# Kernel tuning notes

Hardware: AMD Instinct MI355X
Metric: run time of the kernel (lower is better)

The kernel has to match this reference:

```python
import jax, jax.numpy as jnp
import numpy as np

L, C, H, DH, S, N, B = 12, 768, 12, 64, 2, 577, 1
ALT_START, ROPE_START = 0, 0
OUT_LAYERS = (2, 5, 8, 11)
EPS = 1e-6


def _ln(x, w, b):
    m = jnp.mean(x, axis=-1, keepdims=True)
    v = jnp.var(x, axis=-1, keepdims=True)
    return (x - m) * jax.lax.rsqrt(v + EPS) * w + b


def _rms(x, w):
    return x * jax.lax.rsqrt(jnp.mean(x * x, axis=-1, keepdims=True) + EPS) * w


def _rot_half(x):
    h = x.shape[-1] // 2
    return jnp.concatenate([-x[..., h:], x[..., :h]], axis=-1)


def _rope(t, cos, sin):
    # t: [Bf, H, N, DH]; cos/sin: [N, DH] split into y/x halves
    h = t.shape[-1] // 2
    tv, th = t[..., :h], t[..., h:]
    cy, cx = cos[..., :h], cos[..., h:]
    sy, sx = sin[..., :h], sin[..., h:]
    return jnp.concatenate([tv * cy + _rot_half(tv) * sy,
                            th * cx + _rot_half(th) * sx], axis=-1)


def _block(xf, cos, sin, kv, p):
    (qkv_w, qkv_b, qn, kn, pw, pb, g1, g2,
     n1w, n1b, n2w, n2b, f1w, f1b, f2w, f2b) = p
    Bf, Nn, Cc = xf.shape
    h = _ln(xf, n1w, n1b)
    qkv = (jnp.einsum('bnc,oc->bno', h, qkv_w) + qkv_b)
    qkv = qkv.reshape(Bf, Nn, 3, H, DH).transpose(2, 0, 3, 1, 4)
    q, k, v = qkv[0], qkv[1], qkv[2]
    q, k = _rms(q, qn), _rms(k, kn)
    q, k = _rope(q, cos, sin), _rope(k, cos, sin)
    bias = ((1.0 - kv) * (-10000.0))[:, None, None, :]
    scores = jnp.einsum('bhqd,bhkd->bhqk', q, k) / np.sqrt(DH) + bias
    attn = jax.nn.softmax(scores, axis=-1)
    o = jnp.einsum('bhqk,bhkd->bhqd', attn, v).transpose(0, 2, 1, 3).reshape(Bf, Nn, Cc)
    o = jnp.einsum('bnc,oc->bno', o, pw) + pb
    xf = xf + g1 * o
    h2 = _ln(xf, n2w, n2b)
    m = jax.nn.gelu(jnp.einsum('bnc,oc->bno', h2, f1w) + f1b, approximate=False)
    m = jnp.einsum('bnd,od->bno', m, f2w) + f2b
    return xf + g2 * m


def _forward(x, rope_cos_local, rope_sin_local, rope_cos_global, rope_sin_global,
             key_valid_local, key_valid_global, camera_token,
             qkv_w, qkv_b, q_norm_w, k_norm_w, proj_w, proj_b,
             ls1_gamma, ls2_gamma, norm1_w, norm1_b, norm2_w, norm2_b,
             fc1_w, fc1_b, fc2_w, fc2_b, final_norm_w, final_norm_b):
    Bb, Ss, Nn, Cc = x.shape
    stacked = (qkv_w, qkv_b, q_norm_w, k_norm_w, proj_w, proj_b, ls1_gamma,
               ls2_gamma, norm1_w, norm1_b, norm2_w, norm2_b, fc1_w, fc1_b,
               fc2_w, fc2_b)
    local_x = x
    outputs = []
    cam_token_out = None
    max_out = max(OUT_LAYERS)
    for i in range(L):
        if i == ALT_START:
            ref = jnp.broadcast_to(camera_token[:, :1], (Bb, 1, Cc))
            src = jnp.broadcast_to(camera_token[:, 1:], (Bb, Ss - 1, Cc))
            x = x.at[:, :, 0].set(jnp.concatenate([ref, src], axis=1))
        p = tuple(a[i] for a in stacked)
        is_global = (i % 2 == 1)  # alt_start == 0
        if is_global:
            xf = x.reshape(Bb, Ss * Nn, Cc)
            xf = _block(xf, rope_cos_global, rope_sin_global, key_valid_global, p)
            x = xf.reshape(Bb, Ss, Nn, Cc)
        else:
            xf = x.reshape(Bb * Ss, Nn, Cc)
            xf = _block(xf, rope_cos_local, rope_sin_local, key_valid_local, p)
            x = xf.reshape(Bb, Ss, Nn, Cc)
            local_x = x
        if i in OUT_LAYERS:
            out_x = jnp.concatenate([local_x, x], axis=-1)  # cat_token=True
            outputs.append(out_x)
            if i == max_out:
                cam_token_out = out_x[:, :, 0]
    processed = []
    for o in outputs:
        o = jnp.concatenate([o[..., :Cc], _ln(o[..., Cc:], final_norm_w, final_norm_b)], axis=-1)
        o = o[..., 1:, :]  # drop cam/cls token (num_register_tokens=0)
        processed.append(o)
    return (processed[0], processed[1], processed[2], processed[3], cam_token_out)


def setup_inputs() -> dict:
    key = jax.random.key(0)
    ks = iter(jax.random.split(key, 40))
    rn = lambda sh, s=0.02: jax.random.normal(next(ks), sh, dtype=jnp.float32) * s
    two_pi = 2.0 * np.pi
    ang_l = jax.random.uniform(next(ks), (N, DH), dtype=jnp.float32) * two_pi
    ang_g = jax.random.uniform(next(ks), (S * N, DH), dtype=jnp.float32) * two_pi
    kv_l = (jax.random.uniform(next(ks), (B * S, N)) > 0.1).astype(jnp.float32)
    kv_g = (jax.random.uniform(next(ks), (B, S * N)) > 0.1).astype(jnp.float32)
    return {
        'x': rn((B, S, N, C), 1.0),
        'rope_cos_local': jnp.cos(ang_l), 'rope_sin_local': jnp.sin(ang_l),
        'rope_cos_global': jnp.cos(ang_g), 'rope_sin_global': jnp.sin(ang_g),
        'key_valid_local': kv_l, 'key_valid_global': kv_g,
        'camera_token': rn((1, 2, C)),
        'qkv_w': rn((L, 3 * C, C)), 'qkv_b': rn((L, 3 * C)),
        'q_norm_w': jnp.ones((L, DH), jnp.float32),
        'k_norm_w': jnp.ones((L, DH), jnp.float32),
        'proj_w': rn((L, C, C)), 'proj_b': rn((L, C)),
        'ls1_gamma': rn((L, C), 0.1), 'ls2_gamma': rn((L, C), 0.1),
        'norm1_w': jnp.ones((L, C), jnp.float32), 'norm1_b': jnp.zeros((L, C), jnp.float32),
        'norm2_w': jnp.ones((L, C), jnp.float32), 'norm2_b': jnp.zeros((L, C), jnp.float32),
        'fc1_w': rn((L, 4 * C, C)), 'fc1_b': rn((L, 4 * C)),
        'fc2_w': rn((L, C, 4 * C)), 'fc2_b': rn((L, C)),
        'final_norm_w': jnp.ones((C,), jnp.float32),
        'final_norm_b': jnp.zeros((C,), jnp.float32),
    }


def reference(x, rope_cos_local, rope_sin_local, rope_cos_global, rope_sin_global,
              key_valid_local, key_valid_global, camera_token,
              qkv_w, qkv_b, q_norm_w, k_norm_w, proj_w, proj_b,
              ls1_gamma, ls2_gamma, norm1_w, norm1_b, norm2_w, norm2_b,
              fc1_w, fc1_b, fc2_w, fc2_b, final_norm_w, final_norm_b):
    return _forward(x, rope_cos_local, rope_sin_local, rope_cos_global, rope_sin_global,
                    key_valid_local, key_valid_global, camera_token,
                    qkv_w, qkv_b, q_norm_w, k_norm_w, proj_w, proj_b,
                    ls1_gamma, ls2_gamma, norm1_w, norm1_b, norm2_w, norm2_b,
                    fc1_w, fc1_b, fc2_w, fc2_b, final_norm_w, final_norm_b)
```

## Files before the change

### kernel.cpp

```cpp
#include <hip/hip_runtime.h>
#include <hip/hip_bf16.h>
#include <math.h>

typedef __hip_bfloat16 bf16;
typedef __attribute__((ext_vector_type(4))) float floatx4;
typedef __attribute__((ext_vector_type(8))) short shortx8;

#define T_TOK 1154
#define C_DIM 768
#define H_HEADS 12
#define NLOC 577
#define OUT_PER 1769472

#define NQ  1769472ull
#define NP  589824ull
#define NF1 2359296ull
#define NF2 2359296ull
#define NWTOT 7077888ull
#define WQ  0ull
#define WP  1769472ull
#define WF1 2359296ull
#define WF2 4718592ull

static __device__ __forceinline__ float b2f(bf16 v) { return __bfloat162float(v); }
static __device__ __forceinline__ bf16 f2b(float v) { return __float2bfloat16(v); }

static __device__ __forceinline__ void gload16(const bf16* g, short* l) {
    __builtin_amdgcn_global_load_lds(
        (__attribute__((address_space(1))) void*)(void*)g,
        (__attribute__((address_space(3))) void*)(void*)l, 16, 0, 0);
}

__global__ void k_init(const float* __restrict__ xin, const float* __restrict__ cam,
                       float* __restrict__ xF, int total) {
    int idx = blockIdx.x * 256 + threadIdx.x;
    if (idx >= total) return;
    int t = idx / C_DIM, c = idx - t * C_DIM;
    int s = t / NLOC, n = t - s * NLOC;
    float v = (n == 0) ? cam[s * C_DIM + c] : xin[idx];
    xF[idx] = v;
}

__global__ void k_cast(const float* __restrict__ src, bf16* __restrict__ dst, int total) {
    int idx = blockIdx.x * 256 + threadIdx.x;
    if (idx < total) dst[idx] = f2b(src[idx]);
}

__global__ __launch_bounds__(256) void k_wconv_all(
    const float* __restrict__ wq, const float* __restrict__ wp,
    const float* __restrict__ wf1, const float* __restrict__ wf2,
    bf16* __restrict__ dst, int nL) {
    size_t total = (size_t)nL * NWTOT / 8;
    for (size_t i = (size_t)blockIdx.x * 256 + threadIdx.x; i < total;
         i += (size_t)gridDim.x * 256) {
        size_t e = i * 8;
        size_t layer = e / NWTOT, off = e - layer * NWTOT;
        const float* src; size_t o2;
        if (off < WP)       { src = wq  + layer * NQ;  o2 = off; }
        else if (off < WF1) { src = wp  + layer * NP;  o2 = off - WP; }
        else if (off < WF2) { src = wf1 + layer * NF1; o2 = off - WF1; }
        else                { src = wf2 + layer * NF2; o2 = off - WF2; }
        float4 a = *(const float4*)(src + o2);
        float4 b = *(const float4*)(src + o2 + 4);
        bf16 pk[8];
        pk[0] = f2b(a.x); pk[1] = f2b(a.y); pk[2] = f2b(a.z); pk[3] = f2b(a.w);
        pk[4] = f2b(b.x); pk[5] = f2b(b.y); pk[6] = f2b(b.z); pk[7] = f2b(b.w);
        *(shortx8*)(dst + e) = *(shortx8*)pk;
    }
}

__global__ __launch_bounds__(256) void k_ln(const float* __restrict__ xF,
                                            const float* __restrict__ w, const float* __restrict__ b,
                                            bf16* __restrict__ out) {
    int t = blockIdx.x;
    const float* xr = xF + (size_t)t * C_DIM;
    float s = 0.f, s2 = 0.f;
    for (int c = threadIdx.x; c < C_DIM; c += 256) { float v = xr[c]; s += v; s2 += v * v; }
    __shared__ float red[8];
    for (int o = 32; o; o >>= 1) { s += __shfl_xor(s, o, 64); s2 += __shfl_xor(s2, o, 64); }
    int wv = threadIdx.x >> 6;
    if ((threadIdx.x & 63) == 0) { red[wv] = s; red[4 + wv] = s2; }
    __syncthreads();
    s = red[0] + red[1] + red[2] + red[3];
    s2 = red[4] + red[5] + red[6] + red[7];
    float mean = s * (1.0f / C_DIM);
    float var = s2 * (1.0f / C_DIM) - mean * mean;
    if (var < 0.f) var = 0.f;
    float inv = rsqrtf(var + 1e-6f);
    bf16* orow = out + (size_t)t * C_DIM;
    for (int c = threadIdx.x; c < C_DIM; c += 256) {
        float v = (xr[c] - mean) * inv * w[c] + b[c];
        orow[c] = f2b(v);
    }
}

template<int BM, int BN, int MODE>
__global__ __launch_bounds__(256) void k_gemmT(
    const bf16* __restrict__ A, const bf16* __restrict__ Bt,
    const float* __restrict__ bias, const float* __restrict__ gamma,
    bf16* __restrict__ outB, float* __restrict__ xio,
    int M, int N, int K, int mB, int kS) {
    constexpr int FM = BM / 32;
    constexpr int FN = BN / 32;
    __shared__ short At[2][BM * 64];
    __shared__ short Bs[2][BN * 64];
    int nwg = gridDim.x;
    int lid = blockIdx.x;
    int qd = nwg >> 3, rm = nwg & 7;
    int xcd = lid & 7, pos = lid >> 3;
    int lid2 = (xcd < rm ? xcd * (qd + 1) : rm * (qd + 1) + (xcd - rm) * qd) + pos;
    int mI = lid2 % mB;
    int rest = lid2 / mB;
    int nB = N / BN;
    int nI = rest % nB;
    int kI = rest / nB;
    int m0 = mI * BM, n0 = nI * BN;
    int Ksub = K / kS;
    int kOff = kI * Ksub;
    int tid = threadIdx.x;
    int w = tid >> 6, lane = tid & 63;
    int lr = lane & 15, lq = lane >> 4;
    int wm = w & 1, wn = w >> 1;
    int srow = tid >> 3;
    int schk = tid & 7;
    floatx4 acc[FM][FN] = {};

    auto stage = [&](int buf, int k0) {
        #pragma unroll
        for (int j = 0; j < BM / 32; j++) {
            int r = j * 32 + srow;
            int ar = m0 + r; if (ar >= M) ar = M - 1;
            int gs = schk ^ (r & 7);
            gload16(A + (size_t)ar * K + kOff + k0 + gs * 8, &At[buf][r * 64 + schk * 8]);
        }
        #pragma unroll
        for (int j = 0; j < BN / 32; j++) {
            int r = j * 32 + srow;
            int gs = schk ^ (r & 7);
            gload16(Bt + (size_t)(n0 + r) * K + kOff + k0 + gs * 8, &Bs[buf][r * 64 + schk * 8]);
        }
    };

    int nt = Ksub / 64;
    stage(0, 0);
    __syncthreads();
    int cur = 0;
    int rx = lr & 7;
    for (int t = 0; t < nt; ++t) {
        if (t + 1 < nt) stage(cur ^ 1, (t + 1) * 64);
        #pragma unroll
        for (int kk = 0; kk < 2; kk++) {
            shortx8 af[FM], bg[FN];
            #pragma unroll
            for (int mi = 0; mi < FM; mi++) {
                int rowl = wm * (BM / 2) + mi * 16 + lr;
                af[mi] = *(const shortx8*)&At[cur][rowl * 64 + ((kk * 4 + lq) ^ rx) * 8];
            }
            #pragma unroll
            for (int ni = 0; ni < FN; ni++) {
                int rowl = wn * (BN / 2) + ni * 16 + lr;
                bg[ni] = *(const shortx8*)&Bs[cur][rowl * 64 + ((kk * 4 + lq) ^ rx) * 8];
            }
            #pragma unroll
            for (int mi = 0; mi < FM; mi++)
                #pragma unroll
                for (int ni = 0; ni < FN; ni++)
                    acc[mi][ni] = __builtin_amdgcn_mfma_f32_16x16x32_bf16(af[mi], bg[ni], acc[mi][ni], 0, 0, 0);
        }
        __syncthreads();
        cur ^= 1;
    }

    #pragma unroll
    for (int mi = 0; mi < FM; mi++) {
        #pragma unroll
        for (int ni = 0; ni < FN; ni++) {
            int cc = n0 + wn * (BN / 2) + ni * 16 + lr;
            #pragma unroll
            for (int rg = 0; rg < 4; rg++) {
                int rr = m0 + wm * (BM / 2) + mi * 16 + lq * 4 + rg;
                if (rr < M) {
                    float u = acc[mi][ni][rg];
                    if (MODE == 2) {
                        u += (kI == 0) ? bias[cc] : 0.f;
                        float contrib = gamma[cc] * u;
                        if (kS > 1) atomicAdd(&xio[(size_t)rr * N + cc], contrib);
                        else        xio[(size_t)rr * N + cc] += contrib;
                    } else if (MODE == 1) {
                        u += bias[cc];
                        float g = 0.5f * u * (1.0f + erff(u * 0.70710678118f));
                        outB[(size_t)rr * N + cc] = f2b(g);
                    } else {
                        u += bias[cc];
                        outB[(size_t)rr * N + cc] = f2b(u);
                    }
                }
            }
        }
    }
}

__global__ __launch_bounds__(256) void k_qkprep(
    const bf16* __restrict__ qkv,
    const float* __restrict__ qnw, const float* __restrict__ knw,
    const float* __restrict__ ctab, const float* __restrict__ stab, int posMod,
    bf16* __restrict__ qh, bf16* __restrict__ kh, bf16* __restrict__ vh) {
    int gw = blockIdx.x * 4 + (threadIdx.x >> 6);
    int lane = threadIdx.x & 63;
    if (gw >= T_TOK * H_HEADS) return;
    int t = gw / H_HEADS, h = gw - t * H_HEADS;
    size_t base = (size_t)t * 2304 + h * 64 + lane;
    float q = b2f(qkv[base]), k = b2f(qkv[base + 768]), v = b2f(qkv[base + 1536]);
    float sq = q * q, sk = k * k;
    for (int o = 32; o; o >>= 1) { sq += __shfl_xor(sq, o, 64); sk += __shfl_xor(sk, o, 64); }
    q = q * rsqrtf(sq * (1.0f / 64.0f) + 1e-6f) * qnw[lane];
    k = k * rsqrtf(sk * (1.0f / 64.0f) + 1e-6f) * knw[lane];
    int pos = t % posMod;
    float cv = ctab[pos * 64 + lane];
    float sv = stab[pos * 64 + lane];
    float qp = __shfl_xor(q, 16, 64);
    float kp = __shfl_xor(k, 16, 64);
    float sgn = (lane & 16) ? 1.0f : -1.0f;
    float qo = q * cv + sgn * qp * sv;
    float ko = k * cv + sgn * kp * sv;
    size_t oidx = ((size_t)h * T_TOK + t) * 64 + lane;
    qh[oidx] = f2b(qo);
    kh[oidx] = f2b(ko);
    vh[oidx] = f2b(v);
}

__global__ __launch_bounds__(256) void k_attn2(
    const bf16* __restrict__ qh, const bf16* __restrict__ kh, const bf16* __restrict__ vh,
    const float* __restrict__ mask, bf16* __restrict__ out, int nk) {
    __shared__ short Ks[64 * 72];
    __shared__ short Vs[64 * 72];
    __shared__ short Ps[4][16 * 72];
    __shared__ float bias_s[64];
    int h = blockIdx.y;
    int base = blockIdx.z * nk;
    int tid = threadIdx.x;
    int wv = tid >> 6, lane = tid & 63;
    int lr = lane & 15, lq = lane >> 4;
    int q0 = blockIdx.x * 64 + wv * 16;
    shortx8 qf[2];
    {
        int qr = q0 + lr; if (qr >= nk) qr = nk - 1;
        const bf16* qp = qh + ((size_t)h * T_TOK + base + qr) * 64 + lq * 8;
        qf[0] = *(const shortx8*)(qp);
        qf[1] = *(const shortx8*)(qp + 32);
    }
    float mrow[4] = {-3.0e38f, -3.0e38f, -3.0e38f, -3.0e38f};
    float lrow[4] = {0.f, 0.f, 0.f, 0.f};
    floatx4 accO[4] = {};
    short* pbuf = &Ps[wv][0];
    int nkt = (nk + 63) >> 6;
    for (int kt0 = 0; kt0 < nkt; kt0++) {
        int kbase = kt0 * 64;
        __syncthreads();
        for (int idx = tid; idx < 64 * 8; idx += 256) {
            int kr = idx >> 3, seg = idx & 7;
            int gk = kbase + kr;
            shortx8 v = {};
            if (gk < nk) v = *(const shortx8*)(kh + ((size_t)h * T_TOK + base + gk) * 64 + seg * 8);
            *(shortx8*)&Ks[kr * 72 + seg * 8] = v;
        }
        for (int idx = tid; idx < 64 * 8; idx += 256) {
            int kr = idx & 63, seg = idx >> 6;
            int gk = kbase + kr;
            shortx8 v = {};
            if (gk < nk) v = *(const shortx8*)(vh + ((size_t)h * T_TOK + base + gk) * 64 + seg * 8);
            bf16* vb = (bf16*)&v;
            #pragma unroll
            for (int j = 0; j < 8; j++)
                Vs[(seg * 8 + j) * 72 + kr] = *(short*)&vb[j];
        }
        if (tid < 64) {
            int gk = kbase + tid;
            bias_s[tid] = (gk < nk) ? (1.0f - mask[base + gk]) * -10000.0f : -30000.0f;
        }
        __syncthreads();
        floatx4 s[4];
        #pragma unroll
        for (int nt = 0; nt < 4; nt++) {
            floatx4 accS = {};
            shortx8 k0 = *(const shortx8*)&Ks[(nt * 16 + lr) * 72 + lq * 8];
            shortx8 k1 = *(const shortx8*)&Ks[(nt * 16 + lr) * 72 + 32 + lq * 8];
            accS = __builtin_amdgcn_mfma_f32_16x16x32_bf16(qf[0], k0, accS, 0, 0, 0);
            accS = __builtin_amdgcn_mfma_f32_16x16x32_bf16(qf[1], k1, accS, 0, 0, 0);
            s[nt] = accS;
        }
        float tmax[4] = {-3.0e38f, -3.0e38f, -3.0e38f, -3.0e38f};
        #pragma unroll
        for (int nt = 0; nt < 4; nt++) {
            float bv = bias_s[nt * 16 + lr];
            #pragma unroll
            for (int rg = 0; rg < 4; rg++) {
                float sv = s[nt][rg] * 0.125f + bv;
                s[nt][rg] = sv;
                tmax[rg] = fmaxf(tmax[rg], sv);
            }
        }
        #pragma unroll
        for (int rg = 0; rg < 4; rg++) {
            for (int o = 1; o < 16; o <<= 1) tmax[rg] = fmaxf(tmax[rg], __shfl_xor(tmax[rg], o, 16));
        }
        float fac[4], tsum[4] = {0.f, 0.f, 0.f, 0.f};
        #pragma unroll
        for (int rg = 0; rg < 4; rg++) {
            float mn = fmaxf(mrow[rg], tmax[rg]);
            fac[rg] = __expf(mrow[rg] - mn);
            mrow[rg] = mn;
        }
        #pragma unroll
        for (int nt = 0; nt < 4; nt++) {
            #pragma unroll
            for (int rg = 0; rg < 4; rg++) {
                float e = __expf(s[nt][rg] - mrow[rg]);
                s[nt][rg] = e;
                tsum[rg] += e;
            }
        }
        #pragma unroll
        for (int rg = 0; rg < 4; rg++) {
            for (int o = 1; o < 16; o <<= 1) tsum[rg] += __shfl_xor(tsum[rg], o, 16);
            lrow[rg] = lrow[rg] * fac[rg] + tsum[rg];
        }
        #pragma unroll
        for (int dt = 0; dt < 4; dt++)
            #pragma unroll
            for (int rg = 0; rg < 4; rg++) accO[dt][rg] *= fac[rg];
        #pragma unroll
        for (int nt = 0; nt < 4; nt++) {
            #pragma unroll
            for (int rg = 0; rg < 4; rg++) {
                bf16 pv = f2b(s[nt][rg]);
                pbuf[(lq * 4 + rg) * 72 + nt * 16 + lr] = *(short*)&pv;
            }
        }
        #pragma unroll
        for (int ks = 0; ks < 2; ks++) {
            shortx8 pf = *(const shortx8*)&pbuf[lr * 72 + ks * 32 + lq * 8];
            #pragma unroll
            for (int dt = 0; dt < 4; dt++) {
                shortx8 vf = *(const shortx8*)&Vs[(dt * 16 + lr) * 72 + ks * 32 + lq * 8];
                accO[dt] = __builtin_amdgcn_mfma_f32_16x16x32_bf16(pf, vf, accO[dt], 0, 0, 0);
            }
        }
    }
    float invl[4];
    #pragma unroll
    for (int rg = 0; rg < 4; rg++) invl[rg] = 1.0f / lrow[rg];
    #pragma unroll
    for (int rg = 0; rg < 4; rg++) {
        int qr = q0 + lq * 4 + rg;
        if (qr < nk) {
            bf16* orow = out + (size_t)(base + qr) * C_DIM + h * 64 + lr;
            #pragma unroll
            for (int dt = 0; dt < 4; dt++)
                orow[dt * 16] = f2b(accO[dt][rg] * invl[rg]);
        }
    }
}

__global__ __launch_bounds__(256) void k_output(
    const float* __restrict__ xF, const bf16* __restrict__ lxB,
    const float* __restrict__ fw, const float* __restrict__ fb, float* __restrict__ dst) {
    int b = blockIdx.x;
    int s = b / 576, nn = b - s * 576;
    int t = s * NLOC + nn + 1;
    const float* xr = xF + (size_t)t * C_DIM;
    float sum = 0.f, s2 = 0.f;
    for (int c = threadIdx.x; c < C_DIM; c += 256) { float v = xr[c]; sum += v; s2 += v * v; }
    __shared__ float red[8];
    for (int o = 32; o; o >>= 1) { sum += __shfl_xor(sum, o, 64); s2 += __shfl_xor(s2, o, 64); }
    if ((threadIdx.x & 63) == 0) { red[threadIdx.x >> 6] = sum; red[4 + (threadIdx.x >> 6)] = s2; }
    __syncthreads();
    sum = red[0] + red[1] + red[2] + red[3];
    s2 = red[4] + red[5] + red[6] + red[7];
    float mean = sum * (1.0f / C_DIM);
    float var = s2 * (1.0f / C_DIM) - mean * mean;
    if (var < 0.f) var = 0.f;
    float inv = rsqrtf(var + 1e-6f);
    float* orow = dst + (size_t)b * 1536;
    const bf16* lr = lxB + (size_t)t * C_DIM;
    for (int c = threadIdx.x; c < C_DIM; c += 256) {
        orow[c] = b2f(lr[c]);
        float v = (xr[c] - mean) * inv * fw[c] + fb[c];
        orow[768 + c] = v;
    }
}

__global__ void k_cam(const float* __restrict__ xF, const bf16* __restrict__ lxB,
                      float* __restrict__ dst) {
    for (int idx = threadIdx.x; idx < 2 * 1536; idx += 256) {
        int s = idx / 1536, c = idx - s * 1536;
        int t = s * NLOC;
        float v = (c < 768) ? b2f(lxB[(size_t)t * 768 + c]) : xF[(size_t)t * 768 + (c - 768)];
        dst[idx] = v;
    }
}

extern "C" void kernel_launch(void* const* d_in, const int* in_sizes, int n_in,
                              void* d_out, int out_size, void* d_ws, size_t ws_size,
                              hipStream_t stream) {
    const float* xin  = (const float*)d_in[0];
    const float* rcl  = (const float*)d_in[1];
    const float* rsl  = (const float*)d_in[2];
    const float* rcg  = (const float*)d_in[3];
    const float* rsg  = (const float*)d_in[4];
    const float* kvl  = (const float*)d_in[5];
    const float* kvg  = (const float*)d_in[6];
    const float* cam  = (const float*)d_in[7];
    const float* qkvw = (const float*)d_in[8];
    const float* qkvb = (const float*)d_in[9];
    const float* qnw  = (const float*)d_in[10];
    const float* knw  = (const float*)d_in[11];
    const float* pw   = (const float*)d_in[12];
    const float* pb   = (const float*)d_in[13];
    const float* ls1  = (const float*)d_in[14];
    const float* ls2  = (const float*)d_in[15];
    const float* n1w  = (const float*)d_in[16];
    const float* n1b  = (const float*)d_in[17];
    const float* n2w  = (const float*)d_in[18];
    const float* n2b  = (const float*)d_in[19];
    const float* f1w  = (const float*)d_in[20];
    const float* f1b  = (const float*)d_in[21];
    const float* f2w  = (const float*)d_in[22];
    const float* f2b_ = (const float*)d_in[23];
    const float* fnw  = (const float*)d_in[24];
    const float* fnb  = (const float*)d_in[25];

    char* ws = (char*)d_ws;
    const size_t TC = (size_t)T_TOK * C_DIM;
    float* xF  = (float*)ws; ws += TC * 4;
    bf16* bufA = (bf16*)ws;  ws += (size_t)T_TOK * 3072 * 2;
    bf16* qhb  = (bf16*)ws;  ws += TC * 2;
    bf16* khb  = (bf16*)ws;  ws += TC * 2;
    bf16* vhb  = (bf16*)ws;  ws += TC * 2;
    bf16* hbuf = (bf16*)ws;  ws += TC * 2;
    bf16* lxB  = (bf16*)ws;  ws += TC * 2;
    bf16* wAll = (bf16*)ws;
    size_t usedBase = (size_t)(ws - (char*)d_ws);
    bool bigW = ws_size >= usedBase + 12ull * NWTOT * 2ull;
    (void)n_in; (void)in_sizes; (void)out_size;

    float* out_b = (float*)d_out;

    k_init<<<(int)((TC + 255) / 256), 256, 0, stream>>>(xin, cam, xF, (int)TC);
    if (bigW)
        k_wconv_all<<<4096, 256, 0, stream>>>(qkvw, pw, f1w, f2w, wAll, 12);

    int outIdx = 0;
    for (int i = 0; i < 12; i++) {
        bool isGlobal = (i & 1);
        bf16* wL;
        if (bigW) {
            wL = wAll + (size_t)i * NWTOT;
        } else {
            k_wconv_all<<<2048, 256, 0, stream>>>(
                qkvw + (size_t)i * NQ, pw + (size_t)i * NP,
                f1w + (size_t)i * NF1, f2w + (size_t)i * NF2, wAll, 1);
            wL = wAll;
        }
        k_ln<<<T_TOK, 256, 0, stream>>>(xF, n1w + (size_t)i * 768, n1b + (size_t)i * 768, hbuf);
        k_gemmT<64, 64, 3><<<684, 256, 0, stream>>>(hbuf, wL + WQ,
            qkvb + (size_t)i * 2304, nullptr, bufA, nullptr, T_TOK, 2304, 768, 19, 1);
        k_qkprep<<<(T_TOK * H_HEADS) / 4, 256, 0, stream>>>(bufA,
            qnw + (size_t)i * 64, knw + (size_t)i * 64,
            isGlobal ? rcg : rcl, isGlobal ? rsg : rsl, isGlobal ? 1154 : 577,
            qhb, khb, vhb);
        if (isGlobal)
            k_attn2<<<dim3(19, 12, 1), 256, 0, stream>>>(qhb, khb, vhb, kvg, hbuf, 1154);
        else
            k_attn2<<<dim3(10, 12, 2), 256, 0, stream>>>(qhb, khb, vhb, kvl, hbuf, 577);
        k_gemmT<64, 64, 2><<<456, 256, 0, stream>>>(hbuf, wL + WP,
            pb + (size_t)i * 768, ls1 + (size_t)i * 768, nullptr, xF, T_TOK, 768, 768, 19, 2);
        k_ln<<<T_TOK, 256, 0, stream>>>(xF, n2w + (size_t)i * 768, n2b + (size_t)i * 768, hbuf);
        k_gemmT<64, 64, 1><<<912, 256, 0, stream>>>(hbuf, wL + WF1,
            f1b + (size_t)i * 3072, nullptr, bufA, nullptr, T_TOK, 3072, 768, 19, 1);
        k_gemmT<64, 64, 2><<<912, 256, 0, stream>>>(bufA, wL + WF2,
            f2b_ + (size_t)i * 768, ls2 + (size_t)i * 768, nullptr, xF, T_TOK, 768, 3072, 19, 4);

        if (i == 2 || i == 4 || i == 8 || i == 10)
            k_cast<<<(int)((TC + 255) / 256), 256, 0, stream>>>(xF, lxB, (int)TC);

        if (i == 2 || i == 5 || i == 8 || i == 11) {
            k_output<<<1152, 256, 0, stream>>>(xF, lxB, fnw, fnb, out_b + (size_t)outIdx * OUT_PER);
            if (i == 11)
                k_cam<<<1, 256, 0, stream>>>(xF, lxB, out_b + 4ull * OUT_PER);
            outIdx++;
        }
    }
}
```

Baseline: 1.917 ms.

## Fuse QK norm and RoPE into QKV GEMM, prefetch attention K/V, reshape weight conversion

Replaces the separate qkprep kernel with a dedicated QKV GEMM whose epilogue applies bias, per-head RMS norm (cross-warp reduction through shared memory) and RoPE, then writes head-major q/k/v directly. This removes the intermediate bf16 QKV buffer round trip and one launch per layer. The attention kernel now register-prefetches the next K/V tile and mask bias while the current tile is being processed. The weight-conversion kernel is also changed to a 3D grid with one element group per thread, which drops the grid-stride loop and per-element layer/type division.

```diff
diff --git a/kernel.cpp b/kernel.cpp
--- a/kernel.cpp
+++ b/kernel.cpp
@@ -46,27 +46,27 @@
     if (idx < total) dst[idx] = f2b(src[idx]);
 }
 
-__global__ __launch_bounds__(256) void k_wconv_all(
+__global__ __launch_bounds__(256) void k_wconv3(
     const float* __restrict__ wq, const float* __restrict__ wp,
     const float* __restrict__ wf1, const float* __restrict__ wf2,
-    bf16* __restrict__ dst, int nL) {
-    size_t total = (size_t)nL * NWTOT / 8;
-    for (size_t i = (size_t)blockIdx.x * 256 + threadIdx.x; i < total;
-         i += (size_t)gridDim.x * 256) {
-        size_t e = i * 8;
-        size_t layer = e / NWTOT, off = e - layer * NWTOT;
-        const float* src; size_t o2;
-        if (off < WP)       { src = wq  + layer * NQ;  o2 = off; }
-        else if (off < WF1) { src = wp  + layer * NP;  o2 = off - WP; }
-        else if (off < WF2) { src = wf1 + layer * NF1; o2 = off - WF1; }
-        else                { src = wf2 + layer * NF2; o2 = off - WF2; }
-        float4 a = *(const float4*)(src + o2);
-        float4 b = *(const float4*)(src + o2 + 4);
-        bf16 pk[8];
-        pk[0] = f2b(a.x); pk[1] = f2b(a.y); pk[2] = f2b(a.z); pk[3] = f2b(a.w);
-        pk[4] = f2b(b.x); pk[5] = f2b(b.y); pk[6] = f2b(b.z); pk[7] = f2b(b.w);
-        *(shortx8*)(dst + e) = *(shortx8*)pk;
-    }
+    bf16* __restrict__ dst) {
+    int typ = blockIdx.y, layer = blockIdx.z;
+    size_t cnt, off;
+    const float* srcb;
+    if (typ == 0)      { cnt = NQ;  off = WQ;  srcb = wq; }
+    else if (typ == 1) { cnt = NP;  off = WP;  srcb = wp; }
+    else if (typ == 2) { cnt = NF1; off = WF1; srcb = wf1; }
+    else               { cnt = NF2; off = WF2; srcb = wf2; }
+    size_t e = ((size_t)blockIdx.x * 256 + threadIdx.x) * 8;
+    if (e >= cnt) return;
+    const float* src = srcb + (size_t)layer * cnt + e;
+    bf16* d = dst + (size_t)layer * NWTOT + off + e;
+    float4 a = *(const float4*)(src);
+    float4 b = *(const float4*)(src + 4);
+    bf16 pk[8];
+    pk[0] = f2b(a.x); pk[1] = f2b(a.y); pk[2] = f2b(a.z); pk[3] = f2b(a.w);
+    pk[4] = f2b(b.x); pk[5] = f2b(b.y); pk[6] = f2b(b.z); pk[7] = f2b(b.w);
+    *(shortx8*)d = *(shortx8*)pk;
 }
 
 __global__ __launch_bounds__(256) void k_ln(const float* __restrict__ xF,
@@ -200,33 +200,152 @@
     }
 }
 
-__global__ __launch_bounds__(256) void k_qkprep(
-    const bf16* __restrict__ qkv,
+__global__ __launch_bounds__(256) void k_gemmQKV(
+    const bf16* __restrict__ A, const bf16* __restrict__ Bt,
+    const float* __restrict__ bias,
     const float* __restrict__ qnw, const float* __restrict__ knw,
     const float* __restrict__ ctab, const float* __restrict__ stab, int posMod,
-    bf16* __restrict__ qh, bf16* __restrict__ kh, bf16* __restrict__ vh) {
-    int gw = blockIdx.x * 4 + (threadIdx.x >> 6);
-    int lane = threadIdx.x & 63;
-    if (gw >= T_TOK * H_HEADS) return;
-    int t = gw / H_HEADS, h = gw - t * H_HEADS;
-    size_t base = (size_t)t * 2304 + h * 64 + lane;
-    float q = b2f(qkv[base]), k = b2f(qkv[base + 768]), v = b2f(qkv[base + 1536]);
-    float sq = q * q, sk = k * k;
-    for (int o = 32; o; o >>= 1) { sq += __shfl_xor(sq, o, 64); sk += __shfl_xor(sk, o, 64); }
-    q = q * rsqrtf(sq * (1.0f / 64.0f) + 1e-6f) * qnw[lane];
-    k = k * rsqrtf(sk * (1.0f / 64.0f) + 1e-6f) * knw[lane];
-    int pos = t % posMod;
-    float cv = ctab[pos * 64 + lane];
-    float sv = stab[pos * 64 + lane];
-    float qp = __shfl_xor(q, 16, 64);
-    float kp = __shfl_xor(k, 16, 64);
-    float sgn = (lane & 16) ? 1.0f : -1.0f;
-    float qo = q * cv + sgn * qp * sv;
-    float ko = k * cv + sgn * kp * sv;
-    size_t oidx = ((size_t)h * T_TOK + t) * 64 + lane;
-    qh[oidx] = f2b(qo);
-    kh[oidx] = f2b(ko);
-    vh[oidx] = f2b(v);
+    bf16* __restrict__ qh, bf16* __restrict__ kh, bf16* __restrict__ vh,
+    int M, int K) {
+    constexpr int BM = 64, BN = 64, FM = 2, FN = 2;
+    const int N = 2304, mB = 19;
+    __shared__ short At[2][BM * 64];
+    __shared__ short Bs[2][BN * 64];
+    __shared__ float ssqS[2][64];
+    int nwg = gridDim.x;
+    int lid = blockIdx.x;
+    int qd = nwg >> 3, rm = nwg & 7;
+    int xcd = lid & 7, pos = lid >> 3;
+    int lid2 = (xcd < rm ? xcd * (qd + 1) : rm * (qd + 1) + (xcd - rm) * qd) + pos;
+    int mI = lid2 % mB;
+    int nI = lid2 / mB;
+    int m0 = mI * BM, n0 = nI * BN;
+    int tid = threadIdx.x;
+    int w = tid >> 6, lane = tid & 63;
+    int lr = lane & 15, lq = lane >> 4;
+    int wm = w & 1, wn = w >> 1;
+    int srow = tid >> 3, schk = tid & 7;
+    floatx4 acc[FM][FN] = {};
+
+    auto stage = [&](int buf, int k0) {
+        #pragma unroll
+        for (int j = 0; j < BM / 32; j++) {
+            int r = j * 32 + srow;
+            int ar = m0 + r; if (ar >= M) ar = M - 1;
+            int gs = schk ^ (r & 7);
+            gload16(A + (size_t)ar * K + k0 + gs * 8, &At[buf][r * 64 + schk * 8]);
+        }
+        #pragma unroll
+        for (int j = 0; j < BN / 32; j++) {
+            int r = j * 32 + srow;
+            int gs = schk ^ (r & 7);
+            gload16(Bt + (size_t)(n0 + r) * K + k0 + gs * 8, &Bs[buf][r * 64 + schk * 8]);
+        }
+    };
+
+    int nt = K / 64;
+    stage(0, 0);
+    __syncthreads();
+    int cur = 0;
+    int rx = lr & 7;
+    for (int t = 0; t < nt; ++t) {
+        if (t + 1 < nt) stage(cur ^ 1, (t + 1) * 64);
+        #pragma unroll
+        for (int kk = 0; kk < 2; kk++) {
+            shortx8 af[FM], bg[FN];
+            #pragma unroll
+            for (int mi = 0; mi < FM; mi++) {
+                int rowl = wm * 32 + mi * 16 + lr;
+                af[mi] = *(const shortx8*)&At[cur][rowl * 64 + ((kk * 4 + lq) ^ rx) * 8];
+            }
+            #pragma unroll
+            for (int ni = 0; ni < FN; ni++) {
+                int rowl = wn * 32 + ni * 16 + lr;
+                bg[ni] = *(const shortx8*)&Bs[cur][rowl * 64 + ((kk * 4 + lq) ^ rx) * 8];
+            }
+            #pragma unroll
+            for (int mi = 0; mi < FM; mi++)
+                #pragma unroll
+                for (int ni = 0; ni < FN; ni++)
+                    acc[mi][ni] = __builtin_amdgcn_mfma_f32_16x16x32_bf16(af[mi], bg[ni], acc[mi][ni], 0, 0, 0);
+        }
+        __syncthreads();
+        cur ^= 1;
+    }
+
+    int tile6 = n0 >> 6;
+    int typ = tile6 / 12;
+    int hh = tile6 - typ * 12;
+    float u[FM][FN][4];
+    #pragma unroll
+    for (int mi = 0; mi < FM; mi++)
+        #pragma unroll
+        for (int ni = 0; ni < FN; ni++) {
+            int cc = n0 + wn * 32 + ni * 16 + lr;
+            #pragma unroll
+            for (int rg = 0; rg < 4; rg++) u[mi][ni][rg] = acc[mi][ni][rg] + bias[cc];
+        }
+
+    if (typ == 2) {
+        #pragma unroll
+        for (int mi = 0; mi < FM; mi++)
+            #pragma unroll
+            for (int rg = 0; rg < 4; rg++) {
+                int rr = m0 + wm * 32 + mi * 16 + lq * 4 + rg;
+                if (rr < M) {
+                    #pragma unroll
+                    for (int ni = 0; ni < FN; ni++) {
+                        int d = wn * 32 + ni * 16 + lr;
+                        vh[((size_t)hh * T_TOK + rr) * 64 + d] = f2b(u[mi][ni][rg]);
+                    }
+                }
+            }
+        return;
+    }
+
+    float sq[FM][4];
+    #pragma unroll
+    for (int mi = 0; mi < FM; mi++)
+        #pragma unroll
+        for (int rg = 0; rg < 4; rg++) {
+            float s = u[mi][0][rg] * u[mi][0][rg] + u[mi][1][rg] * u[mi][1][rg];
+            for (int o = 1; o < 16; o <<= 1) s += __shfl_xor(s, o, 16);
+            sq[mi][rg] = s;
+        }
+    if (lr == 0) {
+        #pragma unroll
+        for (int mi = 0; mi < FM; mi++)
+            #pragma unroll
+            for (int rg = 0; rg < 4; rg++)
+                ssqS[wn][wm * 32 + mi * 16 + lq * 4 + rg] = sq[mi][rg];
+    }
+    __syncthreads();
+    const float* wt = (typ == 0) ? qnw : knw;
+    bf16* dstp = (typ == 0) ? qh : kh;
+    int d0 = wn * 32 + lr;
+    int d1 = d0 + 16;
+    float w0 = wt[d0], w1 = wt[d1];
+    #pragma unroll
+    for (int mi = 0; mi < FM; mi++) {
+        #pragma unroll
+        for (int rg = 0; rg < 4; rg++) {
+            int rowl = wm * 32 + mi * 16 + lq * 4 + rg;
+            int rr = m0 + rowl;
+            if (rr >= M) continue;
+            float ssq = ssqS[0][rowl] + ssqS[1][rowl];
+            float rinv = rsqrtf(ssq * (1.0f / 64.0f) + 1e-6f);
+            float n0v = u[mi][0][rg] * rinv * w0;
+            float n1v = u[mi][1][rg] * rinv * w1;
+            int p = (rr >= posMod) ? rr - posMod : rr;
+            float c0 = ctab[p * 64 + d0], s0 = stab[p * 64 + d0];
+            float c1 = ctab[p * 64 + d1], s1 = stab[p * 64 + d1];
+            float o0 = n0v * c0 - n1v * s0;
+            float o1 = n1v * c1 + n0v * s1;
+            size_t ob = ((size_t)hh * T_TOK + rr) * 64;
+            dstp[ob + d0] = f2b(o0);
+            dstp[ob + d1] = f2b(o1);
+        }
+    }
 }
 
 __global__ __launch_bounds__(256) void k_attn2(
@@ -249,35 +368,50 @@
         qf[0] = *(const shortx8*)(qp);
         qf[1] = *(const shortx8*)(qp + 32);
     }
+    int kKr[2], kSeg[2], vKr[2], vSeg[2];
+    #pragma unroll
+    for (int c = 0; c < 2; c++) {
+        int idx = tid + c * 256;
+        kKr[c] = idx >> 3; kSeg[c] = idx & 7;
+        vKr[c] = idx & 63; vSeg[c] = idx >> 6;
+    }
+    shortx8 kpre[2], vpre[2];
+    float bpre = 0.f;
+    auto prefetch = [&](int kbase) {
+        #pragma unroll
+        for (int c = 0; c < 2; c++) {
+            int gk = kbase + kKr[c];
+            shortx8 kv = {};
+            if (gk < nk) kv = *(const shortx8*)(kh + ((size_t)h * T_TOK + base + gk) * 64 + kSeg[c] * 8);
+            kpre[c] = kv;
+            int gv = kbase + vKr[c];
+            shortx8 vv = {};
+            if (gv < nk) vv = *(const shortx8*)(vh + ((size_t)h * T_TOK + base + gv) * 64 + vSeg[c] * 8);
+            vpre[c] = vv;
+        }
+        if (tid < 64) {
+            int gk = kbase + tid;
+            bpre = (gk < nk) ? (1.0f - mask[base + gk]) * -10000.0f : -30000.0f;
+        }
+    };
     float mrow[4] = {-3.0e38f, -3.0e38f, -3.0e38f, -3.0e38f};
     float lrow[4] = {0.f, 0.f, 0.f, 0.f};
     floatx4 accO[4] = {};
     short* pbuf = &Ps[wv][0];
     int nkt = (nk + 63) >> 6;
+    prefetch(0);
     for (int kt0 = 0; kt0 < nkt; kt0++) {
-        int kbase = kt0 * 64;
         __syncthreads();
-        for (int idx = tid; idx < 64 * 8; idx += 256) {
-            int kr = idx >> 3, seg = idx & 7;
-            int gk = kbase + kr;
-            shortx8 v = {};
-            if (gk < nk) v = *(const shortx8*)(kh + ((size_t)h * T_TOK + base + gk) * 64 + seg * 8);
-            *(shortx8*)&Ks[kr * 72 + seg * 8] = v;
-        }
-        for (int idx = tid; idx < 64 * 8; idx += 256) {
-            int kr = idx & 63, seg = idx >> 6;
-            int gk = kbase + kr;
-            shortx8 v = {};
-            if (gk < nk) v = *(const shortx8*)(vh + ((size_t)h * T_TOK + base + gk) * 64 + seg * 8);
-            bf16* vb = (bf16*)&v;
+        #pragma unroll
+        for (int c = 0; c < 2; c++) {
+            *(shortx8*)&Ks[kKr[c] * 72 + kSeg[c] * 8] = kpre[c];
+            bf16* vb = (bf16*)&vpre[c];
             #pragma unroll
             for (int j = 0; j < 8; j++)
-                Vs[(seg * 8 + j) * 72 + kr] = *(short*)&vb[j];
-        }
-        if (tid < 64) {
-            int gk = kbase + tid;
-            bias_s[tid] = (gk < nk) ? (1.0f - mask[base + gk]) * -10000.0f : -30000.0f;
-        }
+                Vs[(vSeg[c] * 8 + j) * 72 + vKr[c]] = *(short*)&vb[j];
+        }
+        if (tid < 64) bias_s[tid] = bpre;
+        if (kt0 + 1 < nkt) prefetch((kt0 + 1) * 64);
         __syncthreads();
         floatx4 s[4];
         #pragma unroll
@@ -448,7 +582,7 @@
 
     k_init<<<(int)((TC + 255) / 256), 256, 0, stream>>>(xin, cam, xF, (int)TC);
     if (bigW)
-        k_wconv_all<<<4096, 256, 0, stream>>>(qkvw, pw, f1w, f2w, wAll, 12);
+        k_wconv3<<<dim3(1152, 4, 12), 256, 0, stream>>>(qkvw, pw, f1w, f2w, wAll);
 
     int outIdx = 0;
     for (int i = 0; i < 12; i++) {
@@ -457,18 +591,17 @@
         if (bigW) {
             wL = wAll + (size_t)i * NWTOT;
         } else {
-            k_wconv_all<<<2048, 256, 0, stream>>>(
+            k_wconv3<<<dim3(1152, 4, 1), 256, 0, stream>>>(
                 qkvw + (size_t)i * NQ, pw + (size_t)i * NP,
-                f1w + (size_t)i * NF1, f2w + (size_t)i * NF2, wAll, 1);
+                f1w + (size_t)i * NF1, f2w + (size_t)i * NF2, wAll);
             wL = wAll;
         }
         k_ln<<<T_TOK, 256, 0, stream>>>(xF, n1w + (size_t)i * 768, n1b + (size_t)i * 768, hbuf);
-        k_gemmT<64, 64, 3><<<684, 256, 0, stream>>>(hbuf, wL + WQ,
-            qkvb + (size_t)i * 2304, nullptr, bufA, nullptr, T_TOK, 2304, 768, 19, 1);
-        k_qkprep<<<(T_TOK * H_HEADS) / 4, 256, 0, stream>>>(bufA,
+        k_gemmQKV<<<684, 256, 0, stream>>>(hbuf, wL + WQ,
+            qkvb + (size_t)i * 2304,
             qnw + (size_t)i * 64, knw + (size_t)i * 64,
             isGlobal ? rcg : rcl, isGlobal ? rsg : rsl, isGlobal ? 1154 : 577,
-            qhb, khb, vhb);
+            qhb, khb, vhb, T_TOK, 768);
         if (isGlobal)
             k_attn2<<<dim3(19, 12, 1), 256, 0, stream>>>(qhb, khb, vhb, kvg, hbuf, 1154);
         else
```

Result: faster. 1.783 ms (-7.0%).
